# Optimization experiments

Hardware: AMD Instinct MI355X
Metric: run time of the kernel (lower is better)

## Reference

```python
import jax, jax.numpy as jnp
import numpy as np

N_NODES = 100000
N_EDGES = 1600000
D_IN = 128
D_OUT = 128
NEG_SLOPE = 0.01  # F.leaky_relu default

def setup_inputs() -> dict:
    key = jax.random.key(0)
    k1, k2, k3, k4, k5, k6 = jax.random.split(key, 6)
    stdv = 1.0 / np.sqrt(D_OUT)
    return {
        "node_features": jax.random.normal(k1, (N_NODES, D_IN), dtype=jnp.float32),
        "edge_row": jax.random.randint(k2, (N_EDGES,), 0, N_NODES),  # dest node per edge
        "edge_col": jax.random.randint(k3, (N_EDGES,), 0, N_NODES),  # src node per edge
        "edge_val": jax.random.uniform(k4, (N_EDGES,), dtype=jnp.float32),
        "weight": jax.random.uniform(k5, (D_IN, D_OUT), dtype=jnp.float32, minval=-stdv, maxval=stdv),
        "bias": jax.random.uniform(k6, (D_OUT,), dtype=jnp.float32, minval=-stdv, maxval=stdv),
    }

def reference(node_features, edge_row, edge_col, edge_val, weight, bias):
    # x = node_features @ W  -> [N, D_OUT]
    h = node_features @ weight
    # spmm(adj, h): gather source features, scale by edge value, scatter-add to dest
    msg = edge_val[:, None] * h[edge_col]                       # [E, D_OUT]
    out = jax.ops.segment_sum(msg, edge_row, num_segments=node_features.shape[0])
    out = out + bias
    out = jnp.where(out >= 0, out, NEG_SLOPE * out)             # leaky_relu
    # dropout p=0 -> identity
    return out
```

## Files before the change

kernel.cpp:

```cpp
#include <hip/hip_runtime.h>

#define DMODEL 128
#define NEG_SLOPE 0.01f
#define NPB 64
#define NBK_MAX 1600
#define CPAD 16
#define NBLK 256
#define SCAP 2048

typedef unsigned int uint;
typedef unsigned short ushort_t;
typedef __attribute__((ext_vector_type(8))) short short8v;
typedef __attribute__((ext_vector_type(4))) float float4v;

__device__ inline ushort_t f2bf(float f) {
    uint u = __float_as_uint(f);
    u += 0x7FFFu + ((u >> 16) & 1u);
    return (ushort_t)(u >> 16);
}

__global__ __launch_bounds__(256) void k_setup(const float* __restrict__ W,
                                               ushort_t* __restrict__ Wt,
                                               int* __restrict__ gcnt_p, int ztot) {
    const int b = blockIdx.x;
    if (b < 64) {
        const int t = b * 256 + threadIdx.x;
        const int k = t >> 7, c = t & 127;
        Wt[(size_t)c * DMODEL + k] = f2bf(W[(size_t)k * DMODEL + c]);
    } else {
        const int i = (b - 64) * 256 + threadIdx.x;
        if (i < ztot) gcnt_p[i] = 0;
    }
}

__global__ __launch_bounds__(256) void k_gemm(const float* __restrict__ X,
                                              const ushort_t* __restrict__ Wt,
                                              ushort_t* __restrict__ H, int N) {
    const int t = threadIdx.x;
    const int wid = t >> 6, lane = t & 63;
    const int wrow = (blockIdx.x * 4 + wid) * 16;
    if (wrow >= N) return;
    const int lr = lane & 15;
    const int kg = lane >> 4;

    const float* xrow = X + (size_t)(wrow + lr) * DMODEL + kg * 8;
    const ushort_t* wtb = Wt + (size_t)lr * DMODEL + kg * 8;

    float4v acc[8] = {};
#pragma unroll
    for (int s = 0; s < 4; ++s) {
        float4 x0 = *(const float4*)(xrow + s * 32);
        float4 x1 = *(const float4*)(xrow + s * 32 + 4);
        short8v af;
        af[0] = (short)f2bf(x0.x); af[1] = (short)f2bf(x0.y);
        af[2] = (short)f2bf(x0.z); af[3] = (short)f2bf(x0.w);
        af[4] = (short)f2bf(x1.x); af[5] = (short)f2bf(x1.y);
        af[6] = (short)f2bf(x1.z); af[7] = (short)f2bf(x1.w);
#pragma unroll
        for (int c = 0; c < 8; ++c) {
            short8v bf = *(const short8v*)(wtb + (size_t)c * 16 * DMODEL + s * 32);
            acc[c] = __builtin_amdgcn_mfma_f32_16x16x32_bf16(af, bf, acc[c], 0, 0, 0);
        }
    }
#pragma unroll
    for (int c = 0; c < 8; ++c) {
#pragma unroll
        for (int r = 0; r < 4; ++r) {
            const int row = wrow + kg * 4 + r;
            H[(size_t)row * DMODEL + c * 16 + lr] = f2bf(acc[c][r]);
        }
    }
}

__global__ __launch_bounds__(1024) void k_bhist(const int* __restrict__ er,
                                                int* __restrict__ gcnt_p,
                                                int* __restrict__ bcnt,
                                                int E, int NBK, int chunk) {
    __shared__ int lh[NBK_MAX];
    const int t = threadIdx.x;
    for (int k = t; k < NBK; k += 1024) lh[k] = 0;
    __syncthreads();
    const int s0 = blockIdx.x * chunk;
    const int s1 = min(E, s0 + chunk);
    for (int i = s0 + t * 4; i < s1; i += 4096) {
        if (i + 3 < s1) {
            int4 r = *(const int4*)(er + i);
            atomicAdd(&lh[r.x >> 6], 1);
            atomicAdd(&lh[r.y >> 6], 1);
            atomicAdd(&lh[r.z >> 6], 1);
            atomicAdd(&lh[r.w >> 6], 1);
        } else {
            for (int q = i; q < s1; ++q) atomicAdd(&lh[er[q] >> 6], 1);
        }
    }
    __syncthreads();
    int* brow = bcnt + (size_t)blockIdx.x * NBK;
    for (int k = t; k < NBK; k += 1024) {
        int c = lh[k];
        brow[k] = c;
        if (c) atomicAdd(&gcnt_p[k * CPAD], c);
    }
}

__global__ __launch_bounds__(256) void k_bscan(const int* __restrict__ gcnt_p,
                                               int* __restrict__ bptr, int NBK) {
    __shared__ int ps[256];
    const int t = threadIdx.x;
    const int SEG = (NBK + 255) >> 8;
    const int base = t * SEG;
    int cnt[16];
    int s = 0;
    for (int i = 0; i < SEG; ++i) {
        int idx = base + i;
        int c = (idx < NBK) ? gcnt_p[idx * CPAD] : 0;
        cnt[i] = c;
        s += c;
    }
    ps[t] = s;
    __syncthreads();
    for (int o = 1; o < 256; o <<= 1) {
        int x = (t >= o) ? ps[t - o] : 0;
        __syncthreads();
        ps[t] += x;
        __syncthreads();
    }
    int run = (t > 0) ? ps[t - 1] : 0;
    for (int i = 0; i < SEG; ++i) {
        int idx = base + i;
        if (idx < NBK) {
            bptr[idx] = run;
            run += cnt[i];
        }
    }
    if (t == 255) bptr[NBK] = ps[255];
}

__global__ __launch_bounds__(64) void k_boff(const int* __restrict__ bcnt,
                                             const int* __restrict__ bptr,
                                             int* __restrict__ boff, int NBK) {
    const int b = blockIdx.x;
    const int l = threadIdx.x;
    int c0 = bcnt[(size_t)(4 * l + 0) * NBK + b];
    int c1 = bcnt[(size_t)(4 * l + 1) * NBK + b];
    int c2 = bcnt[(size_t)(4 * l + 2) * NBK + b];
    int c3 = bcnt[(size_t)(4 * l + 3) * NBK + b];
    int s = c0 + c1 + c2 + c3;
    int ps = s;
    for (int o = 1; o < 64; o <<= 1) {
        int x = __shfl_up(ps, o);
        if (l >= o) ps += x;
    }
    int base = bptr[b] + (ps - s);
    boff[(size_t)(4 * l + 0) * NBK + b] = base;
    boff[(size_t)(4 * l + 1) * NBK + b] = base + c0;
    boff[(size_t)(4 * l + 2) * NBK + b] = base + c0 + c1;
    boff[(size_t)(4 * l + 3) * NBK + b] = base + c0 + c1 + c2;
}

__global__ __launch_bounds__(1024) void k_bscat(const int* __restrict__ er,
                                                const int* __restrict__ ec,
                                                const float* __restrict__ ev,
                                                const int* __restrict__ boff,
                                                int2* __restrict__ packed0,
                                                int E, int NBK, int chunk) {
    __shared__ int lh[NBK_MAX];
    const int t = threadIdx.x;
    const int* brow = boff + (size_t)blockIdx.x * NBK;
    for (int k = t; k < NBK; k += 1024) lh[k] = brow[k];
    __syncthreads();
    const int s0 = blockIdx.x * chunk;
    const int s1 = min(E, s0 + chunk);
    for (int i = s0 + t * 4; i < s1; i += 4096) {
        if (i + 3 < s1) {
            int4 r = *(const int4*)(er + i);
            int4 c = *(const int4*)(ec + i);
            float4 v = *(const float4*)(ev + i);
            int bkt, slot;
            bkt = r.x >> 6; slot = atomicAdd(&lh[bkt], 1);
            packed0[slot] = make_int2(((r.x & 63) << 17) | c.x, __float_as_int(v.x));
            bkt = r.y >> 6; slot = atomicAdd(&lh[bkt], 1);
            packed0[slot] = make_int2(((r.y & 63) << 17) | c.y, __float_as_int(v.y));
            bkt = r.z >> 6; slot = atomicAdd(&lh[bkt], 1);
            packed0[slot] = make_int2(((r.z & 63) << 17) | c.z, __float_as_int(v.z));
            bkt = r.w >> 6; slot = atomicAdd(&lh[bkt], 1);
            packed0[slot] = make_int2(((r.w & 63) << 17) | c.w, __float_as_int(v.w));
        } else {
            for (int q = i; q < s1; ++q) {
                int r = er[q];
                int bkt = r >> 6;
                int slot = atomicAdd(&lh[bkt], 1);
                packed0[slot] = make_int2(((r & 63) << 17) | ec[q], __float_as_int(ev[q]));
            }
        }
    }
}

__global__ __launch_bounds__(512) void k_bagg2(const uint* __restrict__ Hb,
                                               const int* __restrict__ bptr,
                                               const int2* __restrict__ packed0,
                                               const float* __restrict__ bias,
                                               float* __restrict__ out, int N) {
    __shared__ int2 srt[SCAP];
    __shared__ int lcnt[NPB];
    __shared__ int lpref[NPB];
    __shared__ int lcur[NPB];
    const int t = threadIdx.x;
    const int b = blockIdx.x;
    if (t < NPB) { lcnt[t] = 0; lcur[t] = 0; }
    __syncthreads();

    const int s = bptr[b], e = bptr[b + 1];
    const int cnt = e - s;
    const int staged = min(cnt, SCAP);

    int2 myent[4];
#pragma unroll
    for (int k = 0; k < 4; ++k) {
        const int i = t + k * 512;
        myent[k] = make_int2(0, 0);
        if (i < staged) {
            myent[k] = packed0[s + i];
            atomicAdd(&lcnt[((uint)myent[k].x) >> 17], 1);
        }
    }
    __syncthreads();

    if (t < NPB) {
        int p = 0;
        for (int k = 0; k < t; ++k) p += lcnt[k];
        lpref[t] = p;
    }
    __syncthreads();

#pragma unroll
    for (int k = 0; k < 4; ++k) {
        const int i = t + k * 512;
        if (i < staged) {
            const int rl = ((uint)myent[k].x) >> 17;
            const int pos = lpref[rl] + atomicAdd(&lcur[rl], 1);
            srt[pos] = make_int2(myent[k].x & 0x1FFFF, myent[k].y);
        }
    }
    __syncthreads();

    const int wid = t >> 6, lane = t & 63;
    const int h = lane >> 5, sl = lane & 31;
    const float4 bv = ((const float4*)bias)[sl];

    for (int r = wid * 8; r < wid * 8 + 8; ++r) {
        const int node = b * NPB + r;
        if (node >= N) continue;
        const int m = lcnt[r], p0 = lpref[r];
        float4 acc = make_float4(0.f, 0.f, 0.f, 0.f);
        int jj = h;
        for (; jj + 6 < m; jj += 8) {
            const int2 e0 = srt[p0 + jj];
            const int2 e1 = srt[p0 + jj + 2];
            const int2 e2 = srt[p0 + jj + 4];
            const int2 e3 = srt[p0 + jj + 6];
            const uint2 g0 = ((const uint2*)(Hb + (size_t)e0.x * 64))[sl];
            const uint2 g1 = ((const uint2*)(Hb + (size_t)e1.x * 64))[sl];
            const uint2 g2 = ((const uint2*)(Hb + (size_t)e2.x * 64))[sl];
            const uint2 g3 = ((const uint2*)(Hb + (size_t)e3.x * 64))[sl];
            const float v0 = __int_as_float(e0.y);
            const float v1 = __int_as_float(e1.y);
            const float v2 = __int_as_float(e2.y);
            const float v3 = __int_as_float(e3.y);
            acc.x = fmaf(v0, __uint_as_float(g0.x << 16), acc.x);
            acc.y = fmaf(v0, __uint_as_float(g0.x & 0xffff0000u), acc.y);
            acc.z = fmaf(v0, __uint_as_float(g0.y << 16), acc.z);
            acc.w = fmaf(v0, __uint_as_float(g0.y & 0xffff0000u), acc.w);
            acc.x = fmaf(v1, __uint_as_float(g1.x << 16), acc.x);
            acc.y = fmaf(v1, __uint_as_float(g1.x & 0xffff0000u), acc.y);
            acc.z = fmaf(v1, __uint_as_float(g1.y << 16), acc.z);
            acc.w = fmaf(v1, __uint_as_float(g1.y & 0xffff0000u), acc.w);
            acc.x = fmaf(v2, __uint_as_float(g2.x << 16), acc.x);
            acc.y = fmaf(v2, __uint_as_float(g2.x & 0xffff0000u), acc.y);
            acc.z = fmaf(v2, __uint_as_float(g2.y << 16), acc.z);
            acc.w = fmaf(v2, __uint_as_float(g2.y & 0xffff0000u), acc.w);
            acc.x = fmaf(v3, __uint_as_float(g3.x << 16), acc.x);
            acc.y = fmaf(v3, __uint_as_float(g3.x & 0xffff0000u), acc.y);
            acc.z = fmaf(v3, __uint_as_float(g3.y << 16), acc.z);
            acc.w = fmaf(v3, __uint_as_float(g3.y & 0xffff0000u), acc.w);
        }
        for (; jj < m; jj += 2) {
            const int2 e0 = srt[p0 + jj];
            const uint2 g0 = ((const uint2*)(Hb + (size_t)e0.x * 64))[sl];
            const float v0 = __int_as_float(e0.y);
            acc.x = fmaf(v0, __uint_as_float(g0.x << 16), acc.x);
            acc.y = fmaf(v0, __uint_as_float(g0.x & 0xffff0000u), acc.y);
            acc.z = fmaf(v0, __uint_as_float(g0.y << 16), acc.z);
            acc.w = fmaf(v0, __uint_as_float(g0.y & 0xffff0000u), acc.w);
        }
        for (int i = staged; i < cnt; ++i) {
            const int2 en = packed0[s + i];
            if ((int)(((uint)en.x) >> 17) == r && h == 0) {
                const int col = en.x & 0x1FFFF;
                const float v = __int_as_float(en.y);
                const uint2 g = ((const uint2*)(Hb + (size_t)col * 64))[sl];
                acc.x = fmaf(v, __uint_as_float(g.x << 16), acc.x);
                acc.y = fmaf(v, __uint_as_float(g.x & 0xffff0000u), acc.y);
                acc.z = fmaf(v, __uint_as_float(g.y << 16), acc.z);
                acc.w = fmaf(v, __uint_as_float(g.y & 0xffff0000u), acc.w);
            }
        }
        acc.x += __shfl_xor(acc.x, 32);
        acc.y += __shfl_xor(acc.y, 32);
        acc.z += __shfl_xor(acc.z, 32);
        acc.w += __shfl_xor(acc.w, 32);
        if (h == 0) {
            float4 o;
            o.x = acc.x + bv.x; o.y = acc.y + bv.y;
            o.z = acc.z + bv.z; o.w = acc.w + bv.w;
            o.x = o.x >= 0.f ? o.x : NEG_SLOPE * o.x;
            o.y = o.y >= 0.f ? o.y : NEG_SLOPE * o.y;
            o.z = o.z >= 0.f ? o.z : NEG_SLOPE * o.z;
            o.w = o.w >= 0.f ? o.w : NEG_SLOPE * o.w;
            ((float4*)(out + (size_t)node * DMODEL))[sl] = o;
        }
    }
}

extern "C" void kernel_launch(void* const* d_in, const int* in_sizes, int n_in,
                              void* d_out, int out_size, void* d_ws, size_t ws_size,
                              hipStream_t stream) {
    const float* X    = (const float*)d_in[0];
    const int*   er   = (const int*)d_in[1];
    const int*   ec   = (const int*)d_in[2];
    const float* ev   = (const float*)d_in[3];
    const float* W    = (const float*)d_in[4];
    const float* bias = (const float*)d_in[5];
    float* out = (float*)d_out;

    const int N = in_sizes[0] / DMODEL;
    const int E = in_sizes[1];
    const int NBK = (N + NPB - 1) / NPB;

    char* ws = (char*)d_ws;
    size_t off = 0;
    auto alloc = [&](size_t bytes) {
        void* p = ws + off;
        off += (bytes + 127) & ~(size_t)127;
        return p;
    };
    ushort_t* H   = (ushort_t*)alloc((size_t)N * DMODEL * sizeof(ushort_t));
    ushort_t* Wt  = (ushort_t*)alloc((size_t)DMODEL * DMODEL * sizeof(ushort_t));
    int* gcnt_p   = (int*)alloc((size_t)NBK * CPAD * sizeof(int));
    int* bptr     = (int*)alloc((size_t)(NBK + 1) * sizeof(int));
    int* bcnt     = (int*)alloc((size_t)NBLK * NBK * sizeof(int));
    int* boff     = (int*)alloc((size_t)NBLK * NBK * sizeof(int));
    int2* packed0 = (int2*)alloc((size_t)(E + 4) * sizeof(int2));
    (void)ws_size;

    const int ztot = NBK * CPAD;

    hipLaunchKernelGGL(k_setup, dim3(64 + (ztot + 255) / 256), dim3(256), 0, stream,
                       W, Wt, gcnt_p, ztot);
    const int gemm_blocks = (N + 63) / 64;
    hipLaunchKernelGGL(k_gemm, dim3(gemm_blocks), dim3(256), 0, stream, X, Wt, H, N);

    const int chunk = ((((E + NBLK - 1) / NBLK) + 3) & ~3);
    hipLaunchKernelGGL(k_bhist, dim3(NBLK), dim3(1024), 0, stream,
                       er, gcnt_p, bcnt, E, NBK, chunk);
    hipLaunchKernelGGL(k_bscan, dim3(1), dim3(256), 0, stream, gcnt_p, bptr, NBK);
    hipLaunchKernelGGL(k_boff,  dim3(NBK), dim3(64), 0, stream, bcnt, bptr, boff, NBK);
    hipLaunchKernelGGL(k_bscat, dim3(NBLK), dim3(1024), 0, stream,
                       er, ec, ev, boff, packed0, E, NBK, chunk);

    hipLaunchKernelGGL(k_bagg2, dim3(NBK), dim3(512), 0, stream,
                       (const uint*)H, bptr, packed0, bias, out, N);
}
```

Before: 163.2 us.

## Fuse GEMM with single-pass bucket scatter into fixed-capacity slabs

```diff
diff --git a/kernel.cpp b/kernel.cpp
--- a/kernel.cpp
+++ b/kernel.cpp
@@ -5,8 +5,9 @@
 #define NPB 64
 #define NBK_MAX 1600
 #define CPAD 16
-#define NBLK 256
-#define SCAP 2048
+#define SBLK 256
+#define CAP 1536
+#define OCAP 65536
 
 typedef unsigned int uint;
 typedef unsigned short ushort_t;
@@ -19,9 +20,10 @@
     return (ushort_t)(u >> 16);
 }
 
-__global__ __launch_bounds__(256) void k_setup(const float* __restrict__ W,
-                                               ushort_t* __restrict__ Wt,
-                                               int* __restrict__ gcnt_p, int ztot) {
+__global__ __launch_bounds__(256) void k_pre(const float* __restrict__ W,
+                                             ushort_t* __restrict__ Wt,
+                                             int* __restrict__ cur,
+                                             int ztot) {
     const int b = blockIdx.x;
     if (b < 64) {
         const int t = b * 256 + threadIdx.x;
@@ -29,178 +31,125 @@
         Wt[(size_t)c * DMODEL + k] = f2bf(W[(size_t)k * DMODEL + c]);
     } else {
         const int i = (b - 64) * 256 + threadIdx.x;
-        if (i < ztot) gcnt_p[i] = 0;
-    }
-}
-
-__global__ __launch_bounds__(256) void k_gemm(const float* __restrict__ X,
-                                              const ushort_t* __restrict__ Wt,
-                                              ushort_t* __restrict__ H, int N) {
+        if (i < ztot) cur[i] = 0;
+    }
+}
+
+__global__ __launch_bounds__(1024) void k_fused(
+        const int* __restrict__ er, const int* __restrict__ ec,
+        const float* __restrict__ ev, int* __restrict__ cur,
+        int* __restrict__ ocnt, int4* __restrict__ ovf,
+        int2* __restrict__ packed0, int E, int NBK, int chunk,
+        const float* __restrict__ X, const ushort_t* __restrict__ Wt,
+        ushort_t* __restrict__ H, int N) {
+    __shared__ int lh[NBK_MAX];
+    __shared__ int lb[NBK_MAX];
     const int t = threadIdx.x;
-    const int wid = t >> 6, lane = t & 63;
-    const int wrow = (blockIdx.x * 4 + wid) * 16;
-    if (wrow >= N) return;
-    const int lr = lane & 15;
-    const int kg = lane >> 4;
-
-    const float* xrow = X + (size_t)(wrow + lr) * DMODEL + kg * 8;
-    const ushort_t* wtb = Wt + (size_t)lr * DMODEL + kg * 8;
-
-    float4v acc[8] = {};
-#pragma unroll
-    for (int s = 0; s < 4; ++s) {
-        float4 x0 = *(const float4*)(xrow + s * 32);
-        float4 x1 = *(const float4*)(xrow + s * 32 + 4);
-        short8v af;
-        af[0] = (short)f2bf(x0.x); af[1] = (short)f2bf(x0.y);
-        af[2] = (short)f2bf(x0.z); af[3] = (short)f2bf(x0.w);
-        af[4] = (short)f2bf(x1.x); af[5] = (short)f2bf(x1.y);
-        af[6] = (short)f2bf(x1.z); af[7] = (short)f2bf(x1.w);
+
+    if (blockIdx.x < SBLK) {
+        for (int k = t; k < NBK; k += 1024) lh[k] = 0;
+        __syncthreads();
+        const int s0 = blockIdx.x * chunk;
+        const int s1 = min(E, s0 + chunk);
+        for (int i = s0 + t * 4; i < s1; i += 4096) {
+            if (i + 3 < s1) {
+                int4 r = *(const int4*)(er + i);
+                atomicAdd(&lh[r.x >> 6], 1);
+                atomicAdd(&lh[r.y >> 6], 1);
+                atomicAdd(&lh[r.z >> 6], 1);
+                atomicAdd(&lh[r.w >> 6], 1);
+            } else {
+                for (int q = i; q < s1; ++q) atomicAdd(&lh[er[q] >> 6], 1);
+            }
+        }
+        __syncthreads();
+        for (int k = t; k < NBK; k += 1024) {
+            int c = lh[k];
+            lb[k] = c ? atomicAdd(&cur[k * CPAD], c) : 0;
+            lh[k] = 0;
+        }
+        __syncthreads();
+        for (int i = s0 + t * 4; i < s1; i += 4096) {
+            if (i + 3 < s1) {
+                int4 r = *(const int4*)(er + i);
+                int4 c = *(const int4*)(ec + i);
+                float4 v = *(const float4*)(ev + i);
+                int bkt, rl, slot;
+#define SCAT1(RR, CC, VV)                                                     \
+                bkt = (RR) >> 6; rl = (RR) & 63;                              \
+                slot = lb[bkt] + atomicAdd(&lh[bkt], 1);                      \
+                if (slot < CAP)                                               \
+                    packed0[(size_t)bkt * CAP + slot] =                       \
+                        make_int2((rl << 17) | (CC), __float_as_int(VV));     \
+                else {                                                        \
+                    int o = atomicAdd(ocnt, 1);                               \
+                    if (o < OCAP) ovf[o] = make_int4(bkt, rl, (CC), __float_as_int(VV)); \
+                }
+                SCAT1(r.x, c.x, v.x)
+                SCAT1(r.y, c.y, v.y)
+                SCAT1(r.z, c.z, v.z)
+                SCAT1(r.w, c.w, v.w)
+            } else {
+                for (int q = i; q < s1; ++q) {
+                    int rr = er[q];
+                    int bkt = rr >> 6, rl = rr & 63;
+                    int slot = lb[bkt] + atomicAdd(&lh[bkt], 1);
+                    if (slot < CAP)
+                        packed0[(size_t)bkt * CAP + slot] =
+                            make_int2((rl << 17) | ec[q], __float_as_int(ev[q]));
+                    else {
+                        int o = atomicAdd(ocnt, 1);
+                        if (o < OCAP) ovf[o] = make_int4(bkt, rl, ec[q], __float_as_int(ev[q]));
+                    }
+                }
+            }
+        }
+    } else {
+        const int gb = blockIdx.x - SBLK;
+        const int wid = t >> 6, lane = t & 63;
+        const int wrow = (gb * 16 + wid) * 16;
+        if (wrow >= N) return;
+        const int lr = lane & 15;
+        const int kg = lane >> 4;
+
+        const float* xrow = X + (size_t)(wrow + lr) * DMODEL + kg * 8;
+        const ushort_t* wtb = Wt + (size_t)lr * DMODEL + kg * 8;
+
+        float4v acc[8] = {};
+#pragma unroll
+        for (int s = 0; s < 4; ++s) {
+            float4 x0 = *(const float4*)(xrow + s * 32);
+            float4 x1 = *(const float4*)(xrow + s * 32 + 4);
+            short8v af;
+            af[0] = (short)f2bf(x0.x); af[1] = (short)f2bf(x0.y);
+            af[2] = (short)f2bf(x0.z); af[3] = (short)f2bf(x0.w);
+            af[4] = (short)f2bf(x1.x); af[5] = (short)f2bf(x1.y);
+            af[6] = (short)f2bf(x1.z); af[7] = (short)f2bf(x1.w);
+#pragma unroll
+            for (int c = 0; c < 8; ++c) {
+                short8v bf = *(const short8v*)(wtb + (size_t)c * 16 * DMODEL + s * 32);
+                acc[c] = __builtin_amdgcn_mfma_f32_16x16x32_bf16(af, bf, acc[c], 0, 0, 0);
+            }
+        }
 #pragma unroll
         for (int c = 0; c < 8; ++c) {
-            short8v bf = *(const short8v*)(wtb + (size_t)c * 16 * DMODEL + s * 32);
-            acc[c] = __builtin_amdgcn_mfma_f32_16x16x32_bf16(af, bf, acc[c], 0, 0, 0);
-        }
-    }
-#pragma unroll
-    for (int c = 0; c < 8; ++c) {
-#pragma unroll
-        for (int r = 0; r < 4; ++r) {
-            const int row = wrow + kg * 4 + r;
-            H[(size_t)row * DMODEL + c * 16 + lr] = f2bf(acc[c][r]);
-        }
-    }
-}
-
-__global__ __launch_bounds__(1024) void k_bhist(const int* __restrict__ er,
-                                                int* __restrict__ gcnt_p,
-                                                int* __restrict__ bcnt,
-                                                int E, int NBK, int chunk) {
-    __shared__ int lh[NBK_MAX];
-    const int t = threadIdx.x;
-    for (int k = t; k < NBK; k += 1024) lh[k] = 0;
-    __syncthreads();
-    const int s0 = blockIdx.x * chunk;
-    const int s1 = min(E, s0 + chunk);
-    for (int i = s0 + t * 4; i < s1; i += 4096) {
-        if (i + 3 < s1) {
-            int4 r = *(const int4*)(er + i);
-            atomicAdd(&lh[r.x >> 6], 1);
-            atomicAdd(&lh[r.y >> 6], 1);
-            atomicAdd(&lh[r.z >> 6], 1);
-            atomicAdd(&lh[r.w >> 6], 1);
-        } else {
-            for (int q = i; q < s1; ++q) atomicAdd(&lh[er[q] >> 6], 1);
-        }
-    }
-    __syncthreads();
-    int* brow = bcnt + (size_t)blockIdx.x * NBK;
-    for (int k = t; k < NBK; k += 1024) {
-        int c = lh[k];
-        brow[k] = c;
-        if (c) atomicAdd(&gcnt_p[k * CPAD], c);
-    }
-}
-
-__global__ __launch_bounds__(256) void k_bscan(const int* __restrict__ gcnt_p,
-                                               int* __restrict__ bptr, int NBK) {
-    __shared__ int ps[256];
-    const int t = threadIdx.x;
-    const int SEG = (NBK + 255) >> 8;
-    const int base = t * SEG;
-    int cnt[16];
-    int s = 0;
-    for (int i = 0; i < SEG; ++i) {
-        int idx = base + i;
-        int c = (idx < NBK) ? gcnt_p[idx * CPAD] : 0;
-        cnt[i] = c;
-        s += c;
-    }
-    ps[t] = s;
-    __syncthreads();
-    for (int o = 1; o < 256; o <<= 1) {
-        int x = (t >= o) ? ps[t - o] : 0;
-        __syncthreads();
-        ps[t] += x;
-        __syncthreads();
-    }
-    int run = (t > 0) ? ps[t - 1] : 0;
-    for (int i = 0; i < SEG; ++i) {
-        int idx = base + i;
-        if (idx < NBK) {
-            bptr[idx] = run;
-            run += cnt[i];
-        }
-    }
-    if (t == 255) bptr[NBK] = ps[255];
-}
-
-__global__ __launch_bounds__(64) void k_boff(const int* __restrict__ bcnt,
-                                             const int* __restrict__ bptr,
-                                             int* __restrict__ boff, int NBK) {
-    const int b = blockIdx.x;
-    const int l = threadIdx.x;
-    int c0 = bcnt[(size_t)(4 * l + 0) * NBK + b];
-    int c1 = bcnt[(size_t)(4 * l + 1) * NBK + b];
-    int c2 = bcnt[(size_t)(4 * l + 2) * NBK + b];
-    int c3 = bcnt[(size_t)(4 * l + 3) * NBK + b];
-    int s = c0 + c1 + c2 + c3;
-    int ps = s;
-    for (int o = 1; o < 64; o <<= 1) {
-        int x = __shfl_up(ps, o);
-        if (l >= o) ps += x;
-    }
-    int base = bptr[b] + (ps - s);
-    boff[(size_t)(4 * l + 0) * NBK + b] = base;
-    boff[(size_t)(4 * l + 1) * NBK + b] = base + c0;
-    boff[(size_t)(4 * l + 2) * NBK + b] = base + c0 + c1;
-    boff[(size_t)(4 * l + 3) * NBK + b] = base + c0 + c1 + c2;
-}
-
-__global__ __launch_bounds__(1024) void k_bscat(const int* __restrict__ er,
-                                                const int* __restrict__ ec,
-                                                const float* __restrict__ ev,
-                                                const int* __restrict__ boff,
-                                                int2* __restrict__ packed0,
-                                                int E, int NBK, int chunk) {
-    __shared__ int lh[NBK_MAX];
-    const int t = threadIdx.x;
-    const int* brow = boff + (size_t)blockIdx.x * NBK;
-    for (int k = t; k < NBK; k += 1024) lh[k] = brow[k];
-    __syncthreads();
-    const int s0 = blockIdx.x * chunk;
-    const int s1 = min(E, s0 + chunk);
-    for (int i = s0 + t * 4; i < s1; i += 4096) {
-        if (i + 3 < s1) {
-            int4 r = *(const int4*)(er + i);
-            int4 c = *(const int4*)(ec + i);
-            float4 v = *(const float4*)(ev + i);
-            int bkt, slot;
-            bkt = r.x >> 6; slot = atomicAdd(&lh[bkt], 1);
-            packed0[slot] = make_int2(((r.x & 63) << 17) | c.x, __float_as_int(v.x));
-            bkt = r.y >> 6; slot = atomicAdd(&lh[bkt], 1);
-            packed0[slot] = make_int2(((r.y & 63) << 17) | c.y, __float_as_int(v.y));
-            bkt = r.z >> 6; slot = atomicAdd(&lh[bkt], 1);
-            packed0[slot] = make_int2(((r.z & 63) << 17) | c.z, __float_as_int(v.z));
-            bkt = r.w >> 6; slot = atomicAdd(&lh[bkt], 1);
-            packed0[slot] = make_int2(((r.w & 63) << 17) | c.w, __float_as_int(v.w));
-        } else {
-            for (int q = i; q < s1; ++q) {
-                int r = er[q];
-                int bkt = r >> 6;
-                int slot = atomicAdd(&lh[bkt], 1);
-                packed0[slot] = make_int2(((r & 63) << 17) | ec[q], __float_as_int(ev[q]));
-            }
-        }
-    }
-}
-
-__global__ __launch_bounds__(512) void k_bagg2(const uint* __restrict__ Hb,
-                                               const int* __restrict__ bptr,
+#pragma unroll
+            for (int r = 0; r < 4; ++r) {
+                const int row = wrow + kg * 4 + r;
+                H[(size_t)row * DMODEL + c * 16 + lr] = f2bf(acc[c][r]);
+            }
+        }
+    }
+}
+
+__global__ __launch_bounds__(256) void k_bagg2(const uint* __restrict__ Hb,
+                                               const int* __restrict__ cur,
+                                               const int* __restrict__ ocnt,
+                                               const int4* __restrict__ ovf,
                                                const int2* __restrict__ packed0,
                                                const float* __restrict__ bias,
                                                float* __restrict__ out, int N) {
-    __shared__ int2 srt[SCAP];
+    __shared__ int2 srt[CAP];
     __shared__ int lcnt[NPB];
     __shared__ int lpref[NPB];
     __shared__ int lcur[NPB];
@@ -209,17 +158,17 @@
     if (t < NPB) { lcnt[t] = 0; lcur[t] = 0; }
     __syncthreads();
 
-    const int s = bptr[b], e = bptr[b + 1];
-    const int cnt = e - s;
-    const int staged = min(cnt, SCAP);
-
-    int2 myent[4];
-#pragma unroll
-    for (int k = 0; k < 4; ++k) {
-        const int i = t + k * 512;
+    const int cnt = cur[b * CPAD];
+    const int staged = min(cnt, CAP);
+    const int2* slab = packed0 + (size_t)b * CAP;
+
+    int2 myent[6];
+#pragma unroll
+    for (int k = 0; k < 6; ++k) {
+        const int i = t + k * 256;
         myent[k] = make_int2(0, 0);
         if (i < staged) {
-            myent[k] = packed0[s + i];
+            myent[k] = slab[i];
             atomicAdd(&lcnt[((uint)myent[k].x) >> 17], 1);
         }
     }
@@ -233,8 +182,8 @@
     __syncthreads();
 
 #pragma unroll
-    for (int k = 0; k < 4; ++k) {
-        const int i = t + k * 512;
+    for (int k = 0; k < 6; ++k) {
+        const int i = t + k * 256;
         if (i < staged) {
             const int rl = ((uint)myent[k].x) >> 17;
             const int pos = lpref[rl] + atomicAdd(&lcur[rl], 1);
@@ -246,8 +195,9 @@
     const int wid = t >> 6, lane = t & 63;
     const int h = lane >> 5, sl = lane & 31;
     const float4 bv = ((const float4*)bias)[sl];
-
-    for (int r = wid * 8; r < wid * 8 + 8; ++r) {
+    const int oc = min(*ocnt, OCAP);
+
+    for (int r = wid * 16; r < wid * 16 + 16; ++r) {
         const int node = b * NPB + r;
         if (node >= N) continue;
         const int m = lcnt[r], p0 = lpref[r];
@@ -292,12 +242,11 @@
             acc.z = fmaf(v0, __uint_as_float(g0.y << 16), acc.z);
             acc.w = fmaf(v0, __uint_as_float(g0.y & 0xffff0000u), acc.w);
         }
-        for (int i = staged; i < cnt; ++i) {
-            const int2 en = packed0[s + i];
-            if ((int)(((uint)en.x) >> 17) == r && h == 0) {
-                const int col = en.x & 0x1FFFF;
-                const float v = __int_as_float(en.y);
-                const uint2 g = ((const uint2*)(Hb + (size_t)col * 64))[sl];
+        for (int i = 0; i < oc; ++i) {
+            const int4 o4 = ovf[i];
+            if (o4.x == b && o4.y == r && h == 0) {
+                const float v = __int_as_float(o4.w);
+                const uint2 g = ((const uint2*)(Hb + (size_t)o4.z * 64))[sl];
                 acc.x = fmaf(v, __uint_as_float(g.x << 16), acc.x);
                 acc.y = fmaf(v, __uint_as_float(g.x & 0xffff0000u), acc.y);
                 acc.z = fmaf(v, __uint_as_float(g.y << 16), acc.z);
@@ -345,28 +294,23 @@
     };
     ushort_t* H   = (ushort_t*)alloc((size_t)N * DMODEL * sizeof(ushort_t));
     ushort_t* Wt  = (ushort_t*)alloc((size_t)DMODEL * DMODEL * sizeof(ushort_t));
-    int* gcnt_p   = (int*)alloc((size_t)NBK * CPAD * sizeof(int));
-    int* bptr     = (int*)alloc((size_t)(NBK + 1) * sizeof(int));
-    int* bcnt     = (int*)alloc((size_t)NBLK * NBK * sizeof(int));
-    int* boff     = (int*)alloc((size_t)NBLK * NBK * sizeof(int));
-    int2* packed0 = (int2*)alloc((size_t)(E + 4) * sizeof(int2));
+    int* cur      = (int*)alloc(((size_t)NBK * CPAD + 1) * sizeof(int));
+    int* ocnt     = cur + (size_t)NBK * CPAD;
+    int4* ovf     = (int4*)alloc((size_t)OCAP * sizeof(int4));
+    int2* packed0 = (int2*)alloc((size_t)NBK * CAP * sizeof(int2));
     (void)ws_size;
 
-    const int ztot = NBK * CPAD;
-
-    hipLaunchKernelGGL(k_setup, dim3(64 + (ztot + 255) / 256), dim3(256), 0, stream,
-                       W, Wt, gcnt_p, ztot);
-    const int gemm_blocks = (N + 63) / 64;
-    hipLaunchKernelGGL(k_gemm, dim3(gemm_blocks), dim3(256), 0, stream, X, Wt, H, N);
-
-    const int chunk = ((((E + NBLK - 1) / NBLK) + 3) & ~3);
-    hipLaunchKernelGGL(k_bhist, dim3(NBLK), dim3(1024), 0, stream,
-                       er, gcnt_p, bcnt, E, NBK, chunk);
-    hipLaunchKernelGGL(k_bscan, dim3(1), dim3(256), 0, stream, gcnt_p, bptr, NBK);
-    hipLaunchKernelGGL(k_boff,  dim3(NBK), dim3(64), 0, stream, bcnt, bptr, boff, NBK);
-    hipLaunchKernelGGL(k_bscat, dim3(NBLK), dim3(1024), 0, stream,
-                       er, ec, ev, boff, packed0, E, NBK, chunk);
-
-    hipLaunchKernelGGL(k_bagg2, dim3(NBK), dim3(512), 0, stream,
-                       (const uint*)H, bptr, packed0, bias, out, N);
-}
+    const int ztot = NBK * CPAD + 1;
+
+    hipLaunchKernelGGL(k_pre, dim3(64 + (ztot + 255) / 256), dim3(256), 0, stream,
+                       W, Wt, cur, ztot);
+
+    const int chunk = ((((E + SBLK - 1) / SBLK) + 3) & ~3);
+    const int gemm_blocks = (N + 255) / 256;
+    hipLaunchKernelGGL(k_fused, dim3(SBLK + gemm_blocks), dim3(1024), 0, stream,
+                       er, ec, ev, cur, ocnt, ovf, packed0, E, NBK, chunk,
+                       X, Wt, H, N);
+
+    hipLaunchKernelGGL(k_bagg2, dim3(NBK), dim3(256), 0, stream,
+                       (const uint*)H, cur, ocnt, ovf, packed0, bias, out, N);
+}
```

Result: faster. 149.6 us (-8.3%).
